# Kernel optimization log

Hardware: AMD Instinct MI355X
Metric: run time of the kernel (lower is better)

## Reference

```python
import jax, jax.numpy as jnp
import numpy as np

B, STATE_DIM, T = 4096, 24, 8
V, D, LAT = 65536, 64, 128
NL, NH, MAXDIM, MEM = 3, 8, 32, 10
FF = 4 * LAT  # dim_feedforward = latent_dim * 4 = 512


def setup_inputs():
    key = jax.random.key(0)
    ks = jax.random.split(key, 20)
    w = lambda i, shape, s=0.02: (jax.random.normal(ks[i], shape, jnp.float32) * s)
    return {
        "dimension_tokens": jax.random.randint(ks[0], (STATE_DIM, T), 0, V),
        "dimension_traits": jax.random.normal(ks[1], (B, STATE_DIM, 2), jnp.float32),
        "rel_goal": jax.random.normal(ks[2], (B, STATE_DIM), jnp.float32),
        "memory_context": jax.random.normal(ks[3], (B, MEM, D), jnp.float32),
        "token_embedding": w(4, (V, D), 1.0),
        "dim_embedding": w(5, (MAXDIM, D), 1.0),
        "trait_W": w(6, (D, 2)), "trait_b": jnp.zeros((D,), jnp.float32),
        "intent_W": w(7, (D, 1)), "intent_b": jnp.zeros((D,), jnp.float32),
        "cls_token": w(8, (1, 1, D), 1.0),
        "Wqkv": w(9, (NL, 3 * D, D)), "bqkv": jnp.zeros((NL, 3 * D), jnp.float32),
        "Wo": w(10, (NL, D, D)), "bo": jnp.zeros((NL, D), jnp.float32),
        "ln1_g": jnp.ones((NL, D), jnp.float32), "ln1_b": jnp.zeros((NL, D), jnp.float32),
        "W1": w(11, (NL, FF, D)), "b1": jnp.zeros((NL, FF), jnp.float32),
        "W2": w(12, (NL, D, FF)), "b2": jnp.zeros((NL, D), jnp.float32),
        "ln2_g": jnp.ones((NL, D), jnp.float32), "ln2_b": jnp.zeros((NL, D), jnp.float32),
        "out_W": w(13, (LAT, D)), "out_b": jnp.zeros((LAT,), jnp.float32),
        "out_ln_g": jnp.ones((LAT,), jnp.float32), "out_ln_b": jnp.zeros((LAT,), jnp.float32),
    }


def _ln(x, g, b, eps=1e-5):
    m = jnp.mean(x, -1, keepdims=True)
    v = jnp.var(x, -1, keepdims=True)
    return (x - m) * jax.lax.rsqrt(v + eps) * g + b


def _mha(x, Wqkv, bqkv, Wo, bo):
    Bb, S, Dd = x.shape
    hd = Dd // NH
    qkv = x @ Wqkv.T + bqkv
    q, k, v = jnp.split(qkv, 3, axis=-1)
    heads = lambda t: t.reshape(Bb, S, NH, hd).transpose(0, 2, 1, 3)
    q, k, v = heads(q), heads(k), heads(v)
    scores = jnp.einsum('bhqd,bhkd->bhqk', q, k) * np.float32(1.0 / np.sqrt(hd))
    attn = jax.nn.softmax(scores, axis=-1)
    out = jnp.einsum('bhqk,bhkd->bhqd', attn, v).transpose(0, 2, 1, 3).reshape(Bb, S, Dd)
    return out @ Wo.T + bo


def reference(dimension_tokens, dimension_traits, rel_goal, memory_context,
              token_embedding, dim_embedding, trait_W, trait_b, intent_W, intent_b,
              cls_token, Wqkv, bqkv, Wo, bo, ln1_g, ln1_b, W1, b1, W2, b2,
              ln2_g, ln2_b, out_W, out_b, out_ln_g, out_ln_b):
    Bb = rel_goal.shape[0]
    state_dim = rel_goal.shape[-1]
    # fused gather + mean-pool over each dimension's token list: [state_dim, D]
    tok = jnp.mean(token_embedding[dimension_tokens], axis=1)
    pos = dim_embedding[:state_dim]                                   # [state_dim, D]
    trait_e = dimension_traits @ trait_W.T + trait_b                  # [B, state_dim, D]
    intent_e = rel_goal[..., None] @ intent_W.T + intent_b            # [B, state_dim, D]
    seq = tok[None] + pos[None] + trait_e + intent_e                  # [B, state_dim, D]
    cls = jnp.broadcast_to(cls_token, (Bb, 1, D))
    x = jnp.concatenate([cls, seq, memory_context], axis=1)           # [B, 1+state_dim+MEM, D]
    # post-LN (norm_first=False) TransformerEncoder, dropout=0 (eval)
    for l in range(NL):
        x = _ln(x + _mha(x, Wqkv[l], bqkv[l], Wo[l], bo[l]), ln1_g[l], ln1_b[l])
        ff = jax.nn.gelu(x @ W1[l].T + b1[l], approximate=False) @ W2[l].T + b2[l]
        x = _ln(x + ff, ln2_g[l], ln2_b[l])
    situation = _ln(x[:, 0] @ out_W.T + out_b, out_ln_g, out_ln_b)    # [B, LAT]
    situation_sequence = x[:, 1:1 + state_dim]                        # [B, state_dim, D]
    cur = jnp.mean(situation_sequence, axis=1, keepdims=True)
    new_memory = jnp.concatenate([memory_context, cur], axis=1)[:, -MEM:]
    return situation, situation_sequence, new_memory
```

## Files before the change

kernel.cpp:

```cpp
#include <hip/hip_runtime.h>

typedef _Float16 f16;
typedef _Float16 f16x2 __attribute__((ext_vector_type(2)));
typedef _Float16 f16x4 __attribute__((ext_vector_type(4)));
typedef _Float16 f16x8 __attribute__((ext_vector_type(8)));
typedef float floatx4 __attribute__((ext_vector_type(4)));

#define MFMA(a, b, c) __builtin_amdgcn_mfma_f32_16x16x32_f16((a), (b), (c), 0, 0, 0)

constexpr int S = 35;
constexpr int NH = 8;
constexpr int NL = 3;
constexpr int G = 2;
constexpr int RP = 80;
constexpr int MT = 5;
constexpr int BUF = RP * 64;
constexpr int SEQOFF = 4096 * 128;
constexpr int MEMOFF = SEQOFF + 4096 * 24 * 64;
constexpr int TOKPOS_OFF = 245760;

__device__ __forceinline__ int sw64(int r, int c) {
    return (r << 6) + ((((c >> 3) ^ r) & 7) << 3) + (c & 7);
}
__device__ __forceinline__ int sw128(int r, int c) {
    return (r << 7) + ((((c >> 3) ^ (r & 7))) << 3) + (c & 7);
}

struct Params {
    const int* tok;
    const float *traits, *relg, *mem, *temb, *demb, *traitW, *traitb, *intentW, *intentb, *cls;
    const float *bqkv, *bo, *ln1g, *ln1b, *b1, *b2, *ln2g, *ln2b;
    const float *outW, *outb, *olng, *olnb;
    const f16 *Wqkv, *Wo, *W1, *W2;
    const float* tokpos;
    float* out;
};

__global__ void cvt_all(const float* __restrict__ wqkv, const float* __restrict__ wo,
                        const float* __restrict__ w1, const float* __restrict__ w2,
                        const int* __restrict__ tok, const float* __restrict__ temb,
                        const float* __restrict__ demb, const float* __restrict__ traitb,
                        const float* __restrict__ intentb, f16* __restrict__ dst) {
    if (blockIdx.x == 240) {
        float* tp = (float*)(dst + TOKPOS_OFF);
        for (int idx = threadIdx.x; idx < 24 * 64; idx += 256) {
            int s = idx >> 6, d = idx & 63;
            float a = 0.f;
#pragma unroll
            for (int t = 0; t < 8; ++t) a += temb[tok[s * 8 + t] * 64 + d];
            tp[idx] = a * 0.125f + demb[idx] + traitb[d] + intentb[d];
        }
        return;
    }
    int i = (blockIdx.x * 256 + threadIdx.x) * 4;
    const float* src;
    int off;
    if (i < 36864)       { src = wqkv; off = 0; }
    else if (i < 49152)  { src = wo;   off = 36864; }
    else if (i < 147456) { src = w1;   off = 49152; }
    else                 { src = w2;   off = 147456; }
    floatx4 v = *(const floatx4*)&src[i - off];
    f16x4 o;
    o[0] = (f16)v[0]; o[1] = (f16)v[1]; o[2] = (f16)v[2]; o[3] = (f16)v[3];
    *(f16x4*)&dst[i] = o;
}

__device__ inline f16x4 pack4(float a, float b, float c, float d) {
    f16x2 lo = __builtin_bit_cast(f16x2, __builtin_amdgcn_cvt_pkrtz(a, b));
    f16x2 hi = __builtin_bit_cast(f16x2, __builtin_amdgcn_cvt_pkrtz(c, d));
    f16x4 r; r[0] = lo[0]; r[1] = lo[1]; r[2] = hi[0]; r[3] = hi[1];
    return r;
}

__device__ inline float gelu_f(float x) {
    float x2 = x * x;
    float u = __builtin_fmaf(x2, 0.044715f, 1.0f);
    float xm = x * -2.302585f;
    float z = __builtin_amdgcn_exp2f(xm * u);
    return x * __builtin_amdgcn_rcpf(1.f + z);
}

__device__ inline void ln_row_sw(const f16* buf, f16* dst, int row, const float* g, const float* bb) {
    float v[64];
    float sum = 0.f, sq = 0.f;
#pragma unroll
    for (int kv = 0; kv < 8; ++kv) {
        f16x8 x8 = *(const f16x8*)&buf[sw64(row, kv * 8)];
#pragma unroll
        for (int e = 0; e < 8; ++e) {
            float f = (float)x8[e];
            v[kv * 8 + e] = f;
            sum += f;
            sq += f * f;
        }
    }
    float mean = sum * (1.f / 64.f);
    float var = sq * (1.f / 64.f) - mean * mean;
    float rs = rsqrtf(var + 1e-5f);
#pragma unroll
    for (int kv = 0; kv < 16; ++kv) {
        floatx4 g4 = *(const floatx4*)&g[kv * 4];
        floatx4 b4 = *(const floatx4*)&bb[kv * 4];
        *(f16x4*)&dst[sw64(row, kv * 4)] =
            pack4((v[kv * 4 + 0] - mean) * rs * g4[0] + b4[0],
                  (v[kv * 4 + 1] - mean) * rs * g4[1] + b4[1],
                  (v[kv * 4 + 2] - mean) * rs * g4[2] + b4[2],
                  (v[kv * 4 + 3] - mean) * rs * g4[3] + b4[3]);
    }
}

__global__ __launch_bounds__(256, 4) void fused_tfm_kernel(Params p) {
    __shared__ __align__(16) f16 xlds[BUF];
    __shared__ __align__(16) f16 scratch[3 * BUF];

    f16* qbuf = scratch;
    f16* kbuf = scratch + BUF;
    f16* vbuf = scratch + 2 * BUF;
    f16* hbuf = scratch;

    const int tid = threadIdx.x;
    const int lane = tid & 63;
    const int w = tid >> 6;
    const int l15 = lane & 15;
    const int quad = lane >> 4;
    const int b0 = blockIdx.x * G;

    for (int idx = tid; idx < G * S * 64; idx += 256) {
        int i = idx / (S * 64);
        int rem = idx - i * S * 64;
        int r = rem >> 6, d = rem & 63;
        int b = b0 + i;
        float v;
        if (r == 0) {
            v = p.cls[d];
        } else if (r <= 24) {
            int s = r - 1;
            v = p.tokpos[s * 64 + d] + p.traits[b * 48 + s * 2] * p.traitW[d * 2]
                + p.traits[b * 48 + s * 2 + 1] * p.traitW[d * 2 + 1]
                + p.relg[b * 24 + s] * p.intentW[d];
        } else {
            v = p.mem[b * 640 + (r - 25) * 64 + d];
        }
        xlds[sw64(i * S + r, d)] = (f16)v;
    }
    for (int idx = tid; idx < (RP - G * S) * 64; idx += 256) {
        int r = G * S + (idx >> 6), d = idx & 63;
        xlds[sw64(r, d)] = (f16)0.f;
    }
    __syncthreads();

#pragma unroll 1
    for (int l = 0; l < NL; ++l) {
        const f16* Wqkv_l = p.Wqkv + l * 192 * 64;
        const float* bqkv_l = p.bqkv + l * 192;
        const f16* Wo_l = p.Wo + l * 64 * 64;
        const float* bo_l = p.bo + l * 64;
        const float* ln1g_l = p.ln1g + l * 64;
        const float* ln1b_l = p.ln1b + l * 64;
        const f16* W1_l = p.W1 + l * 512 * 64;
        const float* b1_l = p.b1 + l * 512;
        const f16* W2_l = p.W2 + l * 64 * 512;
        const float* b2_l = p.b2 + l * 64;
        const float* ln2g_l = p.ln2g + l * 64;
        const float* ln2b_l = p.ln2b + l * 64;

        {
            f16x8 xb[MT][2];
#pragma unroll
            for (int m = 0; m < MT; ++m)
#pragma unroll
                for (int kf = 0; kf < 2; ++kf)
                    xb[m][kf] = *(const f16x8*)&xlds[sw64(m * 16 + l15, kf * 32 + quad * 8)];
#pragma unroll
            for (int nt = w; nt < 12; nt += 4) {
                f16x8 wf0 = *(const f16x8*)&Wqkv_l[(nt * 16 + l15) * 64 + quad * 8];
                f16x8 wf1 = *(const f16x8*)&Wqkv_l[(nt * 16 + l15) * 64 + 32 + quad * 8];
                floatx4 bias4 = *(const floatx4*)&bqkv_l[nt * 16 + quad * 4];
                f16* dst = scratch + (nt >> 2) * BUF;
                int oc = (nt & 3) * 16 + quad * 4;
                floatx4 acc[MT];
#pragma unroll
                for (int m = 0; m < MT; ++m) {
                    acc[m] = {0.f, 0.f, 0.f, 0.f};
                    acc[m] = MFMA(wf0, xb[m][0], acc[m]);
                    acc[m] = MFMA(wf1, xb[m][1], acc[m]);
                }
#pragma unroll
                for (int m = 0; m < MT; ++m) {
                    int row = m * 16 + l15;
                    *(f16x4*)&dst[sw64(row, oc)] =
                        pack4(acc[m][0] + bias4[0], acc[m][1] + bias4[1],
                              acc[m][2] + bias4[2], acc[m][3] + bias4[3]);
                }
            }
        }
        __syncthreads();

        for (int t = tid; t < G * NH * S; t += 256) {
            int i = t / (NH * S);
            int rem = t - i * (NH * S);
            int h = rem / S;
            int q = rem - h * S;
            int rbase = i * S;
            const f16x2* qp = (const f16x2*)&qbuf[sw64(rbase + q, h * 8)];
            f16x2 q0 = qp[0], q1 = qp[1], q2 = qp[2], q3 = qp[3];
            float sc[S];
            float mx = -1e30f;
#pragma unroll
            for (int j = 0; j < S; ++j) {
                const f16x2* kp = (const f16x2*)&kbuf[sw64(rbase + j, h * 8)];
                f16x2 acc2 = q0 * kp[0];
                acc2 = q1 * kp[1] + acc2;
                acc2 = q2 * kp[2] + acc2;
                acc2 = q3 * kp[3] + acc2;
                float s = ((float)acc2[0] + (float)acc2[1]) * 0.51006982f;
                sc[j] = s;
                mx = fmaxf(mx, s);
            }
            float lsum = 0.f;
#pragma unroll
            for (int j = 0; j < S; ++j) {
                sc[j] = __builtin_amdgcn_exp2f(sc[j] - mx);
                lsum += sc[j];
            }
            f16x2 o0 = {0.f, 0.f}, o1 = {0.f, 0.f}, o2 = {0.f, 0.f}, o3 = {0.f, 0.f};
#pragma unroll
            for (int j = 0; j < S; ++j) {
                const f16x2* vp = (const f16x2*)&vbuf[sw64(rbase + j, h * 8)];
                f16 sj = (f16)sc[j];
                f16x2 s2 = {sj, sj};
                o0 = vp[0] * s2 + o0;
                o1 = vp[1] * s2 + o1;
                o2 = vp[2] * s2 + o2;
                o3 = vp[3] * s2 + o3;
            }
            f16 invh = (f16)__builtin_amdgcn_rcpf(lsum);
            f16x2 inv2 = {invh, invh};
            o0 *= inv2; o1 *= inv2; o2 *= inv2; o3 *= inv2;
            f16x8 ov;
            ov[0] = o0[0]; ov[1] = o0[1]; ov[2] = o1[0]; ov[3] = o1[1];
            ov[4] = o2[0]; ov[5] = o2[1]; ov[6] = o3[0]; ov[7] = o3[1];
            *(f16x8*)&qbuf[sw64(rbase + q, h * 8)] = ov;
        }
        __syncthreads();

        {
            f16x8 ab[MT][2];
#pragma unroll
            for (int m = 0; m < MT; ++m)
#pragma unroll
                for (int kf = 0; kf < 2; ++kf)
                    ab[m][kf] = *(const f16x8*)&qbuf[sw64(m * 16 + l15, kf * 32 + quad * 8)];
            f16x8 wf0 = *(const f16x8*)&Wo_l[(w * 16 + l15) * 64 + quad * 8];
            f16x8 wf1 = *(const f16x8*)&Wo_l[(w * 16 + l15) * 64 + 32 + quad * 8];
            int oc = w * 16 + quad * 4;
            floatx4 bo4 = *(const floatx4*)&bo_l[oc];
            floatx4 oacc[MT];
#pragma unroll
            for (int m = 0; m < MT; ++m) {
                oacc[m] = {0.f, 0.f, 0.f, 0.f};
                oacc[m] = MFMA(wf0, ab[m][0], oacc[m]);
                oacc[m] = MFMA(wf1, ab[m][1], oacc[m]);
            }
#pragma unroll
            for (int m = 0; m < MT; ++m) {
                int row = m * 16 + l15;
                f16x4 res = *(const f16x4*)&xlds[sw64(row, oc)];
                *(f16x4*)&vbuf[sw64(row, oc)] =
                    pack4(oacc[m][0] + bo4[0] + (float)res[0],
                          oacc[m][1] + bo4[1] + (float)res[1],
                          oacc[m][2] + bo4[2] + (float)res[2],
                          oacc[m][3] + bo4[3] + (float)res[3]);
            }
        }
        __syncthreads();

        if (tid < G * S) ln_row_sw(vbuf, xlds, tid, ln1g_l, ln1b_l);
        __syncthreads();

        {
            f16x8 a2[MT][2];
#pragma unroll
            for (int m = 0; m < MT; ++m)
#pragma unroll
                for (int kf = 0; kf < 2; ++kf)
                    a2[m][kf] = *(const f16x8*)&xlds[sw64(m * 16 + l15, kf * 32 + quad * 8)];
            floatx4 facc[MT];
#pragma unroll
            for (int m = 0; m < MT; ++m) facc[m] = {0.f, 0.f, 0.f, 0.f};

#pragma unroll 1
            for (int c = 0; c < 4; ++c) {
#pragma unroll
                for (int ntl = w; ntl < 8; ntl += 4) {
                    int gc = c * 128 + ntl * 16;
                    f16x8 w1f0 = *(const f16x8*)&W1_l[(gc + l15) * 64 + quad * 8];
                    f16x8 w1f1 = *(const f16x8*)&W1_l[(gc + l15) * 64 + 32 + quad * 8];
                    floatx4 b14 = *(const floatx4*)&b1_l[gc + quad * 4];
                    int oc = ntl * 16 + quad * 4;
                    floatx4 hacc[MT];
#pragma unroll
                    for (int m = 0; m < MT; ++m) {
                        hacc[m] = {0.f, 0.f, 0.f, 0.f};
                        hacc[m] = MFMA(w1f0, a2[m][0], hacc[m]);
                        hacc[m] = MFMA(w1f1, a2[m][1], hacc[m]);
                    }
#pragma unroll
                    for (int m = 0; m < MT; ++m) {
                        int row = m * 16 + l15;
                        *(f16x4*)&hbuf[sw128(row, oc)] =
                            pack4(gelu_f(hacc[m][0] + b14[0]), gelu_f(hacc[m][1] + b14[1]),
                                  gelu_f(hacc[m][2] + b14[2]), gelu_f(hacc[m][3] + b14[3]));
                    }
                }
                __syncthreads();
                f16x8 w2f[4];
#pragma unroll
                for (int kf = 0; kf < 4; ++kf)
                    w2f[kf] = *(const f16x8*)&W2_l[(w * 16 + l15) * 512 + c * 128 + kf * 32 + quad * 8];
#pragma unroll
                for (int m = 0; m < MT; ++m) {
                    f16x8 h0 = *(const f16x8*)&hbuf[sw128(m * 16 + l15, 0 + quad * 8)];
                    f16x8 h1 = *(const f16x8*)&hbuf[sw128(m * 16 + l15, 32 + quad * 8)];
                    f16x8 h2 = *(const f16x8*)&hbuf[sw128(m * 16 + l15, 64 + quad * 8)];
                    f16x8 h3 = *(const f16x8*)&hbuf[sw128(m * 16 + l15, 96 + quad * 8)];
                    facc[m] = MFMA(w2f[0], h0, facc[m]);
                    facc[m] = MFMA(w2f[1], h1, facc[m]);
                    facc[m] = MFMA(w2f[2], h2, facc[m]);
                    facc[m] = MFMA(w2f[3], h3, facc[m]);
                }
                __syncthreads();
            }

            int oc = w * 16 + quad * 4;
            floatx4 b24 = *(const floatx4*)&b2_l[oc];
#pragma unroll
            for (int m = 0; m < MT; ++m) {
                int row = m * 16 + l15;
                f16x4 res = *(const f16x4*)&xlds[sw64(row, oc)];
                *(f16x4*)&vbuf[sw64(row, oc)] =
                    pack4(facc[m][0] + b24[0] + (float)res[0],
                          facc[m][1] + b24[1] + (float)res[1],
                          facc[m][2] + b24[2] + (float)res[2],
                          facc[m][3] + b24[3] + (float)res[3]);
            }
        }
        __syncthreads();

        if (tid < G * S) ln_row_sw(vbuf, xlds, tid, ln2g_l, ln2b_l);
        __syncthreads();
    }

    float* sitlds = (float*)scratch;
    {
        int i = tid >> 7, j = tid & 127;
        float s = p.outb[j];
#pragma unroll
        for (int kv = 0; kv < 8; ++kv) {
            f16x8 xv = *(const f16x8*)&xlds[sw64(i * S, kv * 8)];
            floatx4 w0 = *(const floatx4*)&p.outW[j * 64 + kv * 8];
            floatx4 w1 = *(const floatx4*)&p.outW[j * 64 + kv * 8 + 4];
#pragma unroll
            for (int e = 0; e < 4; ++e) s += (float)xv[e] * w0[e];
#pragma unroll
            for (int e = 0; e < 4; ++e) s += (float)xv[4 + e] * w1[e];
        }
        sitlds[i * 128 + j] = s;
    }
    __syncthreads();

    if (w < 2) {
        int i = w;
        float v0 = sitlds[i * 128 + lane];
        float v1 = sitlds[i * 128 + 64 + lane];
        float sum = v0 + v1, sq = v0 * v0 + v1 * v1;
#pragma unroll
        for (int off = 32; off >= 1; off >>= 1) {
            sum += __shfl_xor(sum, off, 64);
            sq += __shfl_xor(sq, off, 64);
        }
        float mean = sum * (1.f / 128.f);
        float rs = rsqrtf(sq * (1.f / 128.f) - mean * mean + 1e-5f);
        int b = b0 + i;
        __builtin_nontemporal_store((v0 - mean) * rs * p.olng[lane] + p.olnb[lane],
                                    &p.out[b * 128 + lane]);
        __builtin_nontemporal_store((v1 - mean) * rs * p.olng[64 + lane] + p.olnb[64 + lane],
                                    &p.out[b * 128 + 64 + lane]);
    }

    for (int pp = tid; pp < G * 384; pp += 256) {
        int i = pp / 384;
        int q = pp - i * 384;
        int s = q >> 4, dp = (q & 15) * 4;
        int b = b0 + i;
        f16x4 xv = *(const f16x4*)&xlds[sw64(i * S + 1 + s, dp)];
        floatx4 o = {(float)xv[0], (float)xv[1], (float)xv[2], (float)xv[3]};
        __builtin_nontemporal_store(o, (floatx4*)&p.out[SEQOFF + b * 1536 + s * 64 + dp]);
    }
    for (int pp = tid; pp < G * 144; pp += 256) {
        int i = pp / 144;
        int q = pp - i * 144;
        int mr = q >> 4, dp = (q & 15) * 4;
        int b = b0 + i;
        floatx4 v = *(const floatx4*)&p.mem[b * 640 + (1 + mr) * 64 + dp];
        __builtin_nontemporal_store(v, (floatx4*)&p.out[MEMOFF + b * 640 + mr * 64 + dp]);
    }
    if (tid < G * 64) {
        int i = tid >> 6, d = tid & 63;
        float s = 0.f;
#pragma unroll
        for (int sr = 0; sr < 24; ++sr) s += (float)xlds[sw64(i * S + 1 + sr, d)];
        __builtin_nontemporal_store(s * (1.f / 24.f), &p.out[MEMOFF + (b0 + i) * 640 + 576 + d]);
    }
}

extern "C" void kernel_launch(void* const* d_in, const int* in_sizes, int n_in,
                              void* d_out, int out_size, void* d_ws, size_t ws_size,
                              hipStream_t stream) {
    (void)in_sizes; (void)n_in; (void)out_size; (void)ws_size;

    f16* ws = (f16*)d_ws;
    hipLaunchKernelGGL(cvt_all, dim3(241), dim3(256), 0, stream,
                       (const float*)d_in[11], (const float*)d_in[13],
                       (const float*)d_in[17], (const float*)d_in[19],
                       (const int*)d_in[0], (const float*)d_in[4],
                       (const float*)d_in[5], (const float*)d_in[7],
                       (const float*)d_in[9], ws);

    Params p;
    p.tok = (const int*)d_in[0];
    p.traits = (const float*)d_in[1];
    p.relg = (const float*)d_in[2];
    p.mem = (const float*)d_in[3];
    p.temb = (const float*)d_in[4];
    p.demb = (const float*)d_in[5];
    p.traitW = (const float*)d_in[6];
    p.traitb = (const float*)d_in[7];
    p.intentW = (const float*)d_in[8];
    p.intentb = (const float*)d_in[9];
    p.cls = (const float*)d_in[10];
    p.bqkv = (const float*)d_in[12];
    p.bo = (const float*)d_in[14];
    p.ln1g = (const float*)d_in[15];
    p.ln1b = (const float*)d_in[16];
    p.b1 = (const float*)d_in[18];
    p.b2 = (const float*)d_in[20];
    p.ln2g = (const float*)d_in[21];
    p.ln2b = (const float*)d_in[22];
    p.outW = (const float*)d_in[23];
    p.outb = (const float*)d_in[24];
    p.olng = (const float*)d_in[25];
    p.olnb = (const float*)d_in[26];
    p.Wqkv = ws;
    p.Wo = ws + 36864;
    p.W1 = ws + 49152;
    p.W2 = ws + 147456;
    p.tokpos = (const float*)(ws + TOKPOS_OFF);
    p.out = (float*)d_out;

    hipLaunchKernelGGL(fused_tfm_kernel, dim3(4096 / G), dim3(256), 0, stream, p);
}
```

Before: 431.7 us.

## Register-block attention over five queries per thread and drop max-subtraction pass

Each thread now handles five consecutive queries of one head, so every K and V row read from LDS is reused across five queries. Attention becomes a single pass that exponentiates raw scores without subtracting the row maximum, accumulating the sum and output together. This cuts LDS traffic and the per-query score array. In exchange only 112 of 256 threads are active, register pressure rises, and skipping the max subtraction risks fp16 overflow if scores grow large.

New measurement: 486.9 us. 12.8% more time.

```diff
diff --git a/kernel.cpp b/kernel.cpp
--- a/kernel.cpp
+++ b/kernel.cpp
@@ -196,51 +196,59 @@
         }
         __syncthreads();
 
-        for (int t = tid; t < G * NH * S; t += 256) {
-            int i = t / (NH * S);
-            int rem = t - i * (NH * S);
-            int h = rem / S;
-            int q = rem - h * S;
+        if (tid < G * NH * 7) {
+            int i = tid / 56;
+            int rem = tid - i * 56;
+            int h = rem / 7;
+            int g = rem - h * 7;
             int rbase = i * S;
-            const f16x2* qp = (const f16x2*)&qbuf[sw64(rbase + q, h * 8)];
-            f16x2 q0 = qp[0], q1 = qp[1], q2 = qp[2], q3 = qp[3];
-            float sc[S];
-            float mx = -1e30f;
+            int qr = rbase + g * 5;
+            f16x2 Q[5][4];
+#pragma unroll
+            for (int u = 0; u < 5; ++u) {
+                const f16x2* qp = (const f16x2*)&qbuf[sw64(qr + u, h * 8)];
+                Q[u][0] = qp[0]; Q[u][1] = qp[1]; Q[u][2] = qp[2]; Q[u][3] = qp[3];
+            }
+            float lsum[5] = {0.f, 0.f, 0.f, 0.f, 0.f};
+            f16x2 o[5][4];
+#pragma unroll
+            for (int u = 0; u < 5; ++u)
+#pragma unroll
+                for (int e = 0; e < 4; ++e) o[u][e] = f16x2{0.f, 0.f};
 #pragma unroll
             for (int j = 0; j < S; ++j) {
                 const f16x2* kp = (const f16x2*)&kbuf[sw64(rbase + j, h * 8)];
-                f16x2 acc2 = q0 * kp[0];
-                acc2 = q1 * kp[1] + acc2;
-                acc2 = q2 * kp[2] + acc2;
-                acc2 = q3 * kp[3] + acc2;
-                float s = ((float)acc2[0] + (float)acc2[1]) * 0.51006982f;
-                sc[j] = s;
-                mx = fmaxf(mx, s);
-            }
-            float lsum = 0.f;
-#pragma unroll
-            for (int j = 0; j < S; ++j) {
-                sc[j] = __builtin_amdgcn_exp2f(sc[j] - mx);
-                lsum += sc[j];
-            }
-            f16x2 o0 = {0.f, 0.f}, o1 = {0.f, 0.f}, o2 = {0.f, 0.f}, o3 = {0.f, 0.f};
-#pragma unroll
-            for (int j = 0; j < S; ++j) {
+                f16x2 k0 = kp[0], k1 = kp[1], k2 = kp[2], k3 = kp[3];
                 const f16x2* vp = (const f16x2*)&vbuf[sw64(rbase + j, h * 8)];
-                f16 sj = (f16)sc[j];
-                f16x2 s2 = {sj, sj};
-                o0 = vp[0] * s2 + o0;
-                o1 = vp[1] * s2 + o1;
-                o2 = vp[2] * s2 + o2;
-                o3 = vp[3] * s2 + o3;
-            }
-            f16 invh = (f16)__builtin_amdgcn_rcpf(lsum);
-            f16x2 inv2 = {invh, invh};
-            o0 *= inv2; o1 *= inv2; o2 *= inv2; o3 *= inv2;
-            f16x8 ov;
-            ov[0] = o0[0]; ov[1] = o0[1]; ov[2] = o1[0]; ov[3] = o1[1];
-            ov[4] = o2[0]; ov[5] = o2[1]; ov[6] = o3[0]; ov[7] = o3[1];
-            *(f16x8*)&qbuf[sw64(rbase + q, h * 8)] = ov;
+                f16x2 v0 = vp[0], v1 = vp[1], v2 = vp[2], v3 = vp[3];
+#pragma unroll
+                for (int u = 0; u < 5; ++u) {
+                    f16x2 a2 = Q[u][0] * k0;
+                    a2 = Q[u][1] * k1 + a2;
+                    a2 = Q[u][2] * k2 + a2;
+                    a2 = Q[u][3] * k3 + a2;
+                    float s = ((float)a2[0] + (float)a2[1]) * 0.51006982f;
+                    float e = __builtin_amdgcn_exp2f(s);
+                    lsum[u] += e;
+                    f16 ef = (f16)e;
+                    f16x2 e2 = {ef, ef};
+                    o[u][0] = v0 * e2 + o[u][0];
+                    o[u][1] = v1 * e2 + o[u][1];
+                    o[u][2] = v2 * e2 + o[u][2];
+                    o[u][3] = v3 * e2 + o[u][3];
+                }
+            }
+#pragma unroll
+            for (int u = 0; u < 5; ++u) {
+                f16 invh = (f16)__builtin_amdgcn_rcpf(lsum[u]);
+                f16x2 inv2 = {invh, invh};
+                f16x8 ov;
+                f16x2 t0 = o[u][0] * inv2, t1 = o[u][1] * inv2;
+                f16x2 t2 = o[u][2] * inv2, t3 = o[u][3] * inv2;
+                ov[0] = t0[0]; ov[1] = t0[1]; ov[2] = t1[0]; ov[3] = t1[1];
+                ov[4] = t2[0]; ov[5] = t2[1]; ov[6] = t3[0]; ov[7] = t3[1];
+                *(f16x8*)&qbuf[sw64(qr + u, h * 8)] = ov;
+            }
         }
         __syncthreads();
 
```
